# Optimization experiments

Hardware: AMD Instinct MI355X
Metric: run time of the kernel (lower is better)

## Reference

```python
import jax, jax.numpy as jnp
import numpy as np

N_EMB = 1024
NUM_HEADS = 16
HEAD_DIM = N_EMB // NUM_HEADS
B, T = 4, 2048


def setup_inputs() -> dict:
    key = jax.random.key(0)
    k1, k2, k3, k4, k5 = jax.random.split(key, 5)
    s = 0.02
    return {
        "x": jax.random.normal(k1, (B, T, N_EMB), dtype=jnp.float32),
        "w_qkv": jax.random.normal(k2, (N_EMB, 3 * N_EMB), dtype=jnp.float32) * s,
        "b_qkv": jnp.zeros((3 * N_EMB,), dtype=jnp.float32),
        "w_proj": jax.random.normal(k3, (N_EMB, N_EMB), dtype=jnp.float32) * s,
        "b_proj": jnp.zeros((N_EMB,), dtype=jnp.float32),
    }


def reference(x, w_qkv, b_qkv, w_proj, b_proj):
    Bx, Tx, C = x.shape
    qkv = x @ w_qkv + b_qkv  # [B,T,3C]
    q, k, v = jnp.split(qkv, 3, axis=-1)
    # [B,H,T,D]
    def heads(t):
        return t.reshape(Bx, Tx, NUM_HEADS, HEAD_DIM).transpose(0, 2, 1, 3)
    q, k, v = heads(q), heads(k), heads(v)
    scale = 1.0 / np.sqrt(HEAD_DIM).astype(np.float32)
    att = jnp.einsum('bhqd,bhkd->bhqk', q, k) * scale
    causal = jnp.tril(jnp.ones((Tx, Tx), dtype=bool))
    att = jnp.where(causal[None, None], att, -jnp.inf)
    att = jax.nn.softmax(att, axis=-1)
    # dropout omitted (eval mode / deterministic reference)
    y = jnp.einsum('bhqk,bhkd->bhqd', att, v)
    y = y.transpose(0, 2, 1, 3).reshape(Bx, Tx, C)
    return y @ w_proj + b_proj
```

## Files before the change

### kernel.cpp

```cpp
#include <hip/hip_runtime.h>
#include <hip/hip_bf16.h>

typedef __attribute__((ext_vector_type(8))) short short8;
typedef __attribute__((ext_vector_type(4))) float f32x4;

static __device__ __forceinline__ unsigned short f2bf(float f) {
    unsigned int u = __builtin_bit_cast(unsigned int, f);
    u += 0x7fff + ((u >> 16) & 1);
    return (unsigned short)(u >> 16);
}

static __device__ __forceinline__ float bf2f(unsigned short u) {
    return __builtin_bit_cast(float, (unsigned int)u << 16);
}

static __device__ __forceinline__ void gl_lds16(const unsigned short* g, unsigned short* l) {
    __builtin_amdgcn_global_load_lds(
        (const __attribute__((address_space(1))) unsigned int*)g,
        (__attribute__((address_space(3))) unsigned int*)l, 16, 0, 0);
}

__global__ __launch_bounds__(256) void k_f32_to_bf16(
    const float* __restrict__ in, unsigned short* __restrict__ out, long n)
{
    long i = ((long)blockIdx.x * 256 + threadIdx.x) * 8;
    if (i >= n) return;
    const f32x4 a = *reinterpret_cast<const f32x4*>(in + i);
    const f32x4 b = *reinterpret_cast<const f32x4*>(in + i + 4);
    union { unsigned short u[8]; uint4 v; } o;
    o.u[0] = f2bf(a[0]); o.u[1] = f2bf(a[1]); o.u[2] = f2bf(a[2]); o.u[3] = f2bf(a[3]);
    o.u[4] = f2bf(b[0]); o.u[5] = f2bf(b[1]); o.u[6] = f2bf(b[2]); o.u[7] = f2bf(b[3]);
    *reinterpret_cast<uint4*>(out + i) = o.v;
}

__global__ __launch_bounds__(256) void k_transpose_w(
    const float* __restrict__ w, unsigned short* __restrict__ wt, int K, int N)
{
    __shared__ unsigned short tile[64][72];
    const int k0 = blockIdx.x * 64, n0 = blockIdx.y * 64;
    const int tid = threadIdx.x;
#pragma unroll
    for (int it = 0; it < 4; ++it) {
        int idx = it * 256 + tid;
        int kl = idx >> 4;
        int nl = (idx & 15) * 4;
        f32x4 v = *reinterpret_cast<const f32x4*>(w + (long)(k0 + kl) * N + n0 + nl);
        tile[kl][nl + 0] = f2bf(v[0]);
        tile[kl][nl + 1] = f2bf(v[1]);
        tile[kl][nl + 2] = f2bf(v[2]);
        tile[kl][nl + 3] = f2bf(v[3]);
    }
    __syncthreads();
#pragma unroll
    for (int it = 0; it < 2; ++it) {
        int idx = it * 256 + tid;
        int nl = idx >> 3;
        int c  = (idx & 7) * 8;
        union { unsigned short u[8]; uint4 v; } o;
#pragma unroll
        for (int j = 0; j < 8; ++j) o.u[j] = tile[c + j][nl];
        *reinterpret_cast<uint4*>(wt + (long)(n0 + nl) * K + k0 + c) = o.v;
    }
}

template <int OUTF32>
__global__ __launch_bounds__(256) void k_gemm_bt(
    const unsigned short* __restrict__ A,
    const unsigned short* __restrict__ Bt,
    const float* __restrict__ bias,
    void* __restrict__ Cv, int M, int N, int K)
{
    __shared__ unsigned short As[128][72];
    __shared__ unsigned short Bs[128][72];
    const int tid = threadIdx.x;
    const int m0 = blockIdx.x * 128;
    const int n0 = blockIdx.y * 128;
    const int w = tid >> 6, lane = tid & 63;
    const int wr = (w >> 1) * 64, wc = (w & 1) * 64;
    const int l4 = lane >> 4, l15 = lane & 15;

    f32x4 acc[4][4] = {};
    const int nk = K / 64;
    for (int kt = 0; kt < nk; ++kt) {
        const int k0 = kt * 64;
        __syncthreads();
#pragma unroll
        for (int it = 0; it < 4; ++it) {
            int idx = it * 256 + tid;
            int r = idx >> 3, c = (idx & 7) * 8;
            *reinterpret_cast<uint4*>(&As[r][c]) =
                *reinterpret_cast<const uint4*>(A + (long)(m0 + r) * K + k0 + c);
            *reinterpret_cast<uint4*>(&Bs[r][c]) =
                *reinterpret_cast<const uint4*>(Bt + (long)(n0 + r) * K + k0 + c);
        }
        __syncthreads();
#pragma unroll
        for (int kk = 0; kk < 2; ++kk) {
            short8 af[4], bf[4];
#pragma unroll
            for (int m = 0; m < 4; ++m)
                af[m] = *reinterpret_cast<const short8*>(&As[wr + m * 16 + l15][kk * 32 + l4 * 8]);
#pragma unroll
            for (int n = 0; n < 4; ++n)
                bf[n] = *reinterpret_cast<const short8*>(&Bs[wc + n * 16 + l15][kk * 32 + l4 * 8]);
#pragma unroll
            for (int m = 0; m < 4; ++m)
#pragma unroll
                for (int n = 0; n < 4; ++n)
                    acc[m][n] = __builtin_amdgcn_mfma_f32_16x16x32_bf16(af[m], bf[n], acc[m][n], 0, 0, 0);
        }
    }
#pragma unroll
    for (int n = 0; n < 4; ++n) {
        const int col = n0 + wc + n * 16 + l15;
        const float bv = bias[col];
#pragma unroll
        for (int m = 0; m < 4; ++m) {
            const int row = m0 + wr + m * 16 + l4 * 4;
#pragma unroll
            for (int i = 0; i < 4; ++i) {
                float v = acc[m][n][i] + bv;
                if (OUTF32)
                    reinterpret_cast<float*>(Cv)[(long)(row + i) * N + col] = v;
                else
                    reinterpret_cast<unsigned short*>(Cv)[(long)(row + i) * N + col] = f2bf(v);
            }
        }
    }
}

__global__ __launch_bounds__(256) void k_transpose_v(
    const unsigned short* __restrict__ qkv, unsigned short* __restrict__ vt, int T)
{
    __shared__ unsigned short tile[64][72];
    const int t0 = blockIdx.x * 64, bh = blockIdx.y;
    const int b = bh >> 4, h = bh & 15;
    const int tid = threadIdx.x;
#pragma unroll
    for (int it = 0; it < 2; ++it) {
        int idx = it * 256 + tid;
        int r = idx >> 3, c = (idx & 7) * 8;
        *reinterpret_cast<uint4*>(&tile[r][c]) =
            *reinterpret_cast<const uint4*>(qkv + (long)(b * T + t0 + r) * 3072 + 2048 + h * 64 + c);
    }
    __syncthreads();
#pragma unroll
    for (int it = 0; it < 2; ++it) {
        int idx = it * 256 + tid;
        int d = idx >> 3, c = (idx & 7) * 8;
        union { unsigned short u[8]; uint4 v; } o;
#pragma unroll
        for (int j = 0; j < 8; ++j) o.u[j] = tile[c + j][d];
        *reinterpret_cast<uint4*>(vt + ((long)bh * 64 + d) * T + t0 + c) = o.v;
    }
}

__global__ __launch_bounds__(256, 3) void k_attn(
    const unsigned short* __restrict__ qkv,
    const unsigned short* __restrict__ vt,
    unsigned short* __restrict__ y, int T)
{
    __shared__ __align__(16) unsigned short Kb[2][64][64];
    __shared__ __align__(16) unsigned short Vb[2][64][64];
    __shared__ unsigned short Ps[4][16][64];
    const int nQT = T >> 6;

    int n = blockIdx.x + gridDim.x * blockIdx.y;
    n = (n & 7) * ((gridDim.x * gridDim.y) >> 3) + (n >> 3);
    const int qa = n & 15;
    const int qb = nQT - 1 - qa;
    const int bh = n >> 4;
    const int b = bh >> 4, h = bh & 15;
    const int tid = threadIdx.x, w = tid >> 6, lane = tid & 63;
    const int l4 = lane >> 4, l15 = lane & 15;

    const float SC = 0.125f * 1.44269504f;

    const unsigned short* qpA = qkv + (long)(b * T + qa * 64 + w * 16 + l15) * 3072 + h * 64;
    const unsigned short* qpB = qkv + (long)(b * T + qb * 64 + w * 16 + l15) * 3072 + h * 64;
    short8 qfA[2], qfB[2];
    qfA[0] = *reinterpret_cast<const short8*>(qpA + l4 * 8);
    qfA[1] = *reinterpret_cast<const short8*>(qpA + 32 + l4 * 8);
    qfB[0] = *reinterpret_cast<const short8*>(qpB + l4 * 8);
    qfB[1] = *reinterpret_cast<const short8*>(qpB + 32 + l4 * 8);
#pragma unroll
    for (int kk = 0; kk < 2; ++kk)
#pragma unroll
        for (int j = 0; j < 8; ++j) {
            qfA[kk][j] = (short)f2bf(bf2f((unsigned short)qfA[kk][j]) * SC);
            qfB[kk][j] = (short)f2bf(bf2f((unsigned short)qfB[kk][j]) * SC);
        }

    const int lrow  = lane >> 3;
    const int lslot = (lane & 7) ^ lrow;
    const unsigned short* kg = qkv + (long)b * T * 3072 + 1024 + h * 64 + lslot * 8;
    const unsigned short* vg = vt + (long)bh * 64 * T + lslot * 8;

    auto stage = [&](int buf, int kt) {
#pragma unroll
        for (int i = 0; i < 2; ++i) {
            const int rb = (w * 2 + i) * 8;
            gl_lds16(kg + (long)(kt * 64 + rb + lrow) * 3072, &Kb[buf][rb][0]);
            gl_lds16(vg + (long)(rb + lrow) * T + kt * 64,    &Vb[buf][rb][0]);
        }
    };

    f32x4 oA[4] = {}, oB[4] = {};
    float lsA[4] = {}, lsB[4] = {};
    const int qrow = w * 16 + l4 * 4;
    int cur = 0;

    auto do_tile = [&](const short8 (&qf)[2], f32x4 (&o)[4], float (&ls)[4],
                       bool diag) {
        f32x4 s[4] = {};
#pragma unroll
        for (int kk = 0; kk < 2; ++kk)
#pragma unroll
            for (int c = 0; c < 4; ++c) {
                const int r = c * 16 + l15;
                short8 kf = *reinterpret_cast<const short8*>(
                    &Kb[cur][r][(((kk * 4 + l4) ^ (r & 7)) * 8)]);
                s[c] = __builtin_amdgcn_mfma_f32_16x16x32_bf16(qf[kk], kf, s[c], 0, 0, 0);
            }
#pragma unroll
        for (int c = 0; c < 4; ++c)
#pragma unroll
            for (int i = 0; i < 4; ++i) {
                float p = exp2f(s[c][i]);
                if (diag && (c * 16 + l15 > qrow + i)) p = 0.f;
                ls[i] += p;
                const int pr = l4 * 4 + i;
                Ps[w][pr][(c * 16 + l15) ^ ((pr & 7) << 3)] =
                    (unsigned short)(__builtin_bit_cast(unsigned int, p) >> 16);
            }
#pragma unroll
        for (int kk = 0; kk < 2; ++kk) {
            short8 pf = *reinterpret_cast<const short8*>(
                &Ps[w][l15][(((kk * 4 + l4) ^ (l15 & 7)) * 8)]);
#pragma unroll
            for (int nn = 0; nn < 4; ++nn) {
                const int r = nn * 16 + l15;
                short8 vf = *reinterpret_cast<const short8*>(
                    &Vb[cur][r][(((kk * 4 + l4) ^ (r & 7)) * 8)]);
                o[nn] = __builtin_amdgcn_mfma_f32_16x16x32_bf16(pf, vf, o[nn], 0, 0, 0);
            }
        }
    };

    stage(0, 0);
    __syncthreads();
    for (int kt = 0; kt <= qb; ++kt) {
        if (kt < qb) stage(cur ^ 1, kt + 1);
        do_tile(qfB, oB, lsB, kt == qb);
        if (kt <= qa) do_tile(qfA, oA, lsA, kt == qa);
        __syncthreads();
        cur ^= 1;
    }

#pragma unroll
    for (int i = 0; i < 4; ++i) {
        float la = lsA[i], lb = lsB[i];
#pragma unroll
        for (int off = 1; off < 16; off <<= 1) {
            la += __shfl_xor(la, off);
            lb += __shfl_xor(lb, off);
        }
        float invA = 1.f / la;
        float invB = 1.f / lb;
        int qArow = qa * 64 + w * 16 + l4 * 4 + i;
        int qBrow = qb * 64 + w * 16 + l4 * 4 + i;
        unsigned short* ypA = y + (long)(b * T + qArow) * 1024 + h * 64;
        unsigned short* ypB = y + (long)(b * T + qBrow) * 1024 + h * 64;
#pragma unroll
        for (int nn = 0; nn < 4; ++nn) {
            ypA[nn * 16 + l15] = f2bf(oA[nn][i] * invA);
            ypB[nn * 16 + l15] = f2bf(oB[nn][i] * invB);
        }
    }
}

extern "C" void kernel_launch(void* const* d_in, const int* in_sizes, int n_in,
                              void* d_out, int out_size, void* d_ws, size_t ws_size,
                              hipStream_t stream) {
    const float* x      = (const float*)d_in[0];
    const float* w_qkv  = (const float*)d_in[1];
    const float* b_qkv  = (const float*)d_in[2];
    const float* w_proj = (const float*)d_in[3];
    const float* b_proj = (const float*)d_in[4];
    float* out = (float*)d_out;

    const int B = 4, T = 2048, C = 1024, H = 16;
    const long M = (long)B * T;

    char* ws = (char*)d_ws;
    unsigned short* xb  = (unsigned short*)ws; ws += M * C * 2;
    unsigned short* wqt = (unsigned short*)ws; ws += (long)3 * C * C * 2;
    unsigned short* wpt = (unsigned short*)ws; ws += (long)C * C * 2;
    unsigned short* qkv = (unsigned short*)ws; ws += M * 3 * C * 2;
    unsigned short* vt  = (unsigned short*)ws; ws += M * C * 2;
    unsigned short* y   = (unsigned short*)ws; ws += M * C * 2;

    k_f32_to_bf16<<<(int)((M * C / 8 + 255) / 256), 256, 0, stream>>>(x, xb, M * C);
    {
        dim3 g(C / 64, 3 * C / 64);
        k_transpose_w<<<g, 256, 0, stream>>>(w_qkv, wqt, C, 3 * C);
    }
    {
        dim3 g(C / 64, C / 64);
        k_transpose_w<<<g, 256, 0, stream>>>(w_proj, wpt, C, C);
    }
    {
        dim3 g(M / 128, 3 * C / 128);
        k_gemm_bt<0><<<g, 256, 0, stream>>>(xb, wqt, b_qkv, qkv, (int)M, 3 * C, C);
    }
    {
        dim3 g(T / 64, B * H);
        k_transpose_v<<<g, 256, 0, stream>>>(qkv, vt, T);
    }
    {
        dim3 g(T / 128, B * H);
        k_attn<<<g, 256, 0, stream>>>(qkv, vt, y, T);
    }
    {
        dim3 g(M / 128, C / 128);
        k_gemm_bt<1><<<g, 256, 0, stream>>>(y, wpt, b_proj, out, (int)M, C, C);
    }
}
```

Measured before the change: 212.6 us.

## Use direct-to-LDS swizzled loads in GEMM and share K/V fragments across paired Q tiles

The GEMM now loads A and B tiles with global_load_lds into XOR-swizzled, unpadded shared memory instead of register round-trips, and remaps workgroup IDs so neighbouring blocks are spread across groups of eight. In attention, the two query tiles (A and B) are processed together in each K/V step. Each K and V fragment is read from LDS once and feeds both tiles' MFMAs, with a separate P buffer per tile. This cuts LDS traffic and improves MFMA interleaving, at the cost of more live registers and doubled P shared memory, which may reduce occupancy.

```diff
diff --git a/kernel.cpp b/kernel.cpp
--- a/kernel.cpp
+++ b/kernel.cpp
@@ -70,14 +70,21 @@
     const float* __restrict__ bias,
     void* __restrict__ Cv, int M, int N, int K)
 {
-    __shared__ unsigned short As[128][72];
-    __shared__ unsigned short Bs[128][72];
+    __shared__ __align__(16) unsigned short As[128][64];
+    __shared__ __align__(16) unsigned short Bs[128][64];
     const int tid = threadIdx.x;
-    const int m0 = blockIdx.x * 128;
-    const int n0 = blockIdx.y * 128;
+
+    const int nwg = gridDim.x * gridDim.y;
+    int id = blockIdx.x + gridDim.x * blockIdx.y;
+    id = (id & 7) * (nwg >> 3) + (id >> 3);
+    const int m0 = (id % gridDim.x) * 128;
+    const int n0 = (id / gridDim.x) * 128;
+
     const int w = tid >> 6, lane = tid & 63;
     const int wr = (w >> 1) * 64, wc = (w & 1) * 64;
     const int l4 = lane >> 4, l15 = lane & 15;
+    const int lrow  = lane >> 3;
+    const int lslot = (lane & 7) ^ lrow;
 
     f32x4 acc[4][4] = {};
     const int nk = K / 64;
@@ -86,23 +93,24 @@
         __syncthreads();
 #pragma unroll
         for (int it = 0; it < 4; ++it) {
-            int idx = it * 256 + tid;
-            int r = idx >> 3, c = (idx & 7) * 8;
-            *reinterpret_cast<uint4*>(&As[r][c]) =
-                *reinterpret_cast<const uint4*>(A + (long)(m0 + r) * K + k0 + c);
-            *reinterpret_cast<uint4*>(&Bs[r][c]) =
-                *reinterpret_cast<const uint4*>(Bt + (long)(n0 + r) * K + k0 + c);
+            const int rb = (w * 4 + it) * 8;
+            gl_lds16(A  + (long)(m0 + rb + lrow) * K + k0 + lslot * 8, &As[rb][0]);
+            gl_lds16(Bt + (long)(n0 + rb + lrow) * K + k0 + lslot * 8, &Bs[rb][0]);
         }
         __syncthreads();
 #pragma unroll
         for (int kk = 0; kk < 2; ++kk) {
             short8 af[4], bf[4];
 #pragma unroll
-            for (int m = 0; m < 4; ++m)
-                af[m] = *reinterpret_cast<const short8*>(&As[wr + m * 16 + l15][kk * 32 + l4 * 8]);
-#pragma unroll
-            for (int n = 0; n < 4; ++n)
-                bf[n] = *reinterpret_cast<const short8*>(&Bs[wc + n * 16 + l15][kk * 32 + l4 * 8]);
+            for (int m = 0; m < 4; ++m) {
+                const int r = wr + m * 16 + l15;
+                af[m] = *reinterpret_cast<const short8*>(&As[r][((kk * 4 + l4) ^ (r & 7)) * 8]);
+            }
+#pragma unroll
+            for (int n = 0; n < 4; ++n) {
+                const int r = wc + n * 16 + l15;
+                bf[n] = *reinterpret_cast<const short8*>(&Bs[r][((kk * 4 + l4) ^ (r & 7)) * 8]);
+            }
 #pragma unroll
             for (int m = 0; m < 4; ++m)
 #pragma unroll
@@ -162,7 +170,7 @@
 {
     __shared__ __align__(16) unsigned short Kb[2][64][64];
     __shared__ __align__(16) unsigned short Vb[2][64][64];
-    __shared__ unsigned short Ps[4][16][64];
+    __shared__ unsigned short Ps[4][2][16][64];
     const int nQT = T >> 6;
 
     int n = blockIdx.x + gridDim.x * blockIdx.y;
@@ -210,18 +218,7 @@
     const int qrow = w * 16 + l4 * 4;
     int cur = 0;
 
-    auto do_tile = [&](const short8 (&qf)[2], f32x4 (&o)[4], float (&ls)[4],
-                       bool diag) {
-        f32x4 s[4] = {};
-#pragma unroll
-        for (int kk = 0; kk < 2; ++kk)
-#pragma unroll
-            for (int c = 0; c < 4; ++c) {
-                const int r = c * 16 + l15;
-                short8 kf = *reinterpret_cast<const short8*>(
-                    &Kb[cur][r][(((kk * 4 + l4) ^ (r & 7)) * 8)]);
-                s[c] = __builtin_amdgcn_mfma_f32_16x16x32_bf16(qf[kk], kf, s[c], 0, 0, 0);
-            }
+    auto process = [&](f32x4 (&s)[4], float (&ls)[4], bool diag, int tix) {
 #pragma unroll
         for (int c = 0; c < 4; ++c)
 #pragma unroll
@@ -230,29 +227,48 @@
                 if (diag && (c * 16 + l15 > qrow + i)) p = 0.f;
                 ls[i] += p;
                 const int pr = l4 * 4 + i;
-                Ps[w][pr][(c * 16 + l15) ^ ((pr & 7) << 3)] =
+                Ps[w][tix][pr][(c * 16 + l15) ^ ((pr & 7) << 3)] =
                     (unsigned short)(__builtin_bit_cast(unsigned int, p) >> 16);
             }
+    };
+
+    stage(0, 0);
+    __syncthreads();
+    for (int kt = 0; kt <= qb; ++kt) {
+        if (kt < qb) stage(cur ^ 1, kt + 1);
+        const bool actA = (kt <= qa);
+
+        f32x4 sA[4] = {}, sB[4] = {};
+#pragma unroll
+        for (int kk = 0; kk < 2; ++kk)
+#pragma unroll
+            for (int c = 0; c < 4; ++c) {
+                const int r = c * 16 + l15;
+                short8 kf = *reinterpret_cast<const short8*>(
+                    &Kb[cur][r][(((kk * 4 + l4) ^ (r & 7)) * 8)]);
+                sB[c] = __builtin_amdgcn_mfma_f32_16x16x32_bf16(qfB[kk], kf, sB[c], 0, 0, 0);
+                if (actA) sA[c] = __builtin_amdgcn_mfma_f32_16x16x32_bf16(qfA[kk], kf, sA[c], 0, 0, 0);
+            }
+
+        process(sB, lsB, kt == qb, 0);
+        if (actA) process(sA, lsA, kt == qa, 1);
+
 #pragma unroll
         for (int kk = 0; kk < 2; ++kk) {
-            short8 pf = *reinterpret_cast<const short8*>(
-                &Ps[w][l15][(((kk * 4 + l4) ^ (l15 & 7)) * 8)]);
+            short8 pfB = *reinterpret_cast<const short8*>(
+                &Ps[w][0][l15][(((kk * 4 + l4) ^ (l15 & 7)) * 8)]);
+            short8 pfA;
+            if (actA) pfA = *reinterpret_cast<const short8*>(
+                &Ps[w][1][l15][(((kk * 4 + l4) ^ (l15 & 7)) * 8)]);
 #pragma unroll
             for (int nn = 0; nn < 4; ++nn) {
                 const int r = nn * 16 + l15;
                 short8 vf = *reinterpret_cast<const short8*>(
                     &Vb[cur][r][(((kk * 4 + l4) ^ (r & 7)) * 8)]);
-                o[nn] = __builtin_amdgcn_mfma_f32_16x16x32_bf16(pf, vf, o[nn], 0, 0, 0);
-            }
-        }
-    };
-
-    stage(0, 0);
-    __syncthreads();
-    for (int kt = 0; kt <= qb; ++kt) {
-        if (kt < qb) stage(cur ^ 1, kt + 1);
-        do_tile(qfB, oB, lsB, kt == qb);
-        if (kt <= qa) do_tile(qfA, oA, lsA, kt == qa);
+                oB[nn] = __builtin_amdgcn_mfma_f32_16x16x32_bf16(pfB, vf, oB[nn], 0, 0, 0);
+                if (actA) oA[nn] = __builtin_amdgcn_mfma_f32_16x16x32_bf16(pfA, vf, oA[nn], 0, 0, 0);
+            }
+        }
         __syncthreads();
         cur ^= 1;
     }
```

New measurement: 229.7 us. 8.1% more time.
